# Optimization experiments

Measured on AMD Instinct MI355X. Metric: run time of the kernel, lower is better.

Reference implementation:

```python
import jax, jax.numpy as jnp
import numpy as np

HEADS = 12
WH = WW = 7
N = WH * WW  # 49 tokens per window
NW = 64      # windows per image (mask groups)


def _relative_position_index():
    ch, cw = np.meshgrid(np.arange(WH), np.arange(WW), indexing='ij')
    coords = np.stack([ch, cw]).reshape(2, -1)  # [2, N]
    rel = coords[:, :, None] - coords[:, None, :]  # [2, N, N]
    rel = rel.transpose(1, 2, 0)
    rel[:, :, 0] += WH - 1
    rel[:, :, 1] += WW - 1
    rel[:, :, 0] *= 2 * WW - 1
    return rel.sum(-1).astype(np.int32)  # [N, N]


def setup_inputs() -> dict:
    key = jax.random.key(0)
    ks = jax.random.split(key, 6)
    B, C = 4096, 384
    x = jax.random.normal(ks[0], (B, N, C), dtype=jnp.float32)
    mask = jnp.where(jax.random.uniform(ks[1], (NW, N, N)) > 0.5, 0.0, -100.0).astype(jnp.float32)
    W_qkv = jax.random.normal(ks[2], (C, 3 * C), dtype=jnp.float32) * 0.02
    b_qkv = jnp.zeros((3 * C,), dtype=jnp.float32)
    W_out = jax.random.normal(ks[3], (C, C), dtype=jnp.float32) * 0.02
    b_out = jnp.zeros((C,), dtype=jnp.float32)
    rpb_table = jax.random.normal(ks[4], ((2 * WH - 1) * (2 * WW - 1), HEADS), dtype=jnp.float32) * 0.01
    rel_index = jnp.asarray(_relative_position_index())
    return {"x": x, "mask": mask, "W_qkv": W_qkv, "b_qkv": b_qkv,
            "W_out": W_out, "b_out": b_out, "rpb_table": rpb_table,
            "rel_index": rel_index}


def reference(x, mask, W_qkv, b_qkv, W_out, b_out, rpb_table, rel_index):
    B, n, C = x.shape
    hd = C // HEADS
    scale = hd ** (-0.5)
    qkv = x @ W_qkv + b_qkv                      # [B, n, 3C]
    q, k, v = jnp.split(qkv, 3, axis=2)
    def heads(t):
        return t.reshape(B, n, HEADS, hd).transpose(0, 2, 1, 3)  # b h n d
    q = heads(q) * scale
    k = heads(k)
    v = heads(v)
    attn = jnp.einsum('bhmc,bhnc->bhmn', q, k)   # [B, h, n, n]
    bias = rpb_table[rel_index.reshape(-1)].reshape(n, n, HEADS).transpose(2, 0, 1)
    attn = attn + bias[None]
    nw = mask.shape[0]
    attn = attn.reshape(B // nw, nw, HEADS, n, n) + mask[None, :, None]
    attn = attn.reshape(B, HEADS, n, n)
    attn = jax.nn.softmax(attn, axis=3)
    out = jnp.einsum('bhmn,bhnc->bhmc', attn, v)  # [B, h, n, d]
    out = out.transpose(0, 2, 1, 3).reshape(B, n, C)
    return out @ W_out + b_out
```

## Files before the change

### kernel.cpp

```cpp
#include <hip/hip_runtime.h>

#define NTOK 49
#define CDIM 384
#define HEADS 12
#define HD 32
#define NWIN 64
#define NQKV 1152
#define SCALE 0.17677669529663687f

typedef __attribute__((ext_vector_type(8))) __bf16 bf16x8;
typedef __attribute__((ext_vector_type(4))) float f32x4;

#define OFF_WQKVT   0ull
#define OFF_WOUTT   884736ull
#define OFF_RPBF    1179648ull
#define OFF_MASKF   1376256ull
#define OFF_QKVB    8555520ull
#define OFF_ATTNOUT 470977536ull
#define OFF_XB      OFF_ATTNOUT

#define TSIZE 77070336ull

__device__ __forceinline__ void async_copy16(__bf16* lds_dst, const __bf16* g_src) {
    __builtin_amdgcn_global_load_lds(
        (const __attribute__((address_space(1))) void*)g_src,
        (__attribute__((address_space(3))) void*)lds_dst,
        16, 0, 0);
}


__global__ void prep_weights(const float* __restrict__ Wqkv, const float* __restrict__ Wout,
                             __bf16* __restrict__ WqkvT, __bf16* __restrict__ WoutT) {
    int idx = blockIdx.x * 256 + threadIdx.x;
    if (idx < NQKV * CDIM) {
        int n = idx / CDIM, k = idx % CDIM;
        WqkvT[idx] = (__bf16)Wqkv[(size_t)k * NQKV + n];
    }
    if (idx < CDIM * CDIM) {
        int n = idx / CDIM, k = idx % CDIM;
        WoutT[idx] = (__bf16)Wout[(size_t)k * CDIM + n];
    }
}

__global__ void prep_frag(const float* __restrict__ rpb, const int* __restrict__ rel,
                          const float* __restrict__ mask,
                          float* __restrict__ rpbF, float* __restrict__ maskF) {
    int idx = blockIdx.x * 256 + threadIdx.x;
    if (idx < 49152) {
        int r = idx & 3, lane = (idx >> 2) & 63, nt = (idx >> 8) & 3, mt = (idx >> 10) & 3, h = idx >> 12;
        int m = mt * 16 + ((lane >> 4) << 2) + r, n = nt * 16 + (lane & 15);
        rpbF[idx] = (m < NTOK && n < NTOK) ? rpb[rel[m * NTOK + n] * HEADS + h] : 0.f;
    } else {
        int i2 = idx - 49152;
        if (i2 < 262144) {
            int r = i2 & 3, lane = (i2 >> 2) & 63, nt = (i2 >> 8) & 3, mt = (i2 >> 10) & 3, w = i2 >> 12;
            int m = mt * 16 + ((lane >> 4) << 2) + r, n = nt * 16 + (lane & 15);
            maskF[i2] = (m < NTOK && n < NTOK) ? mask[(size_t)w * NTOK * NTOK + m * NTOK + n] : 0.f;
        }
    }
}

__global__ __launch_bounds__(256) void prep_xb(const float* __restrict__ x,
                                               __bf16* __restrict__ xb, int total8) {
    int stride = gridDim.x * 256;
    for (int i = blockIdx.x * 256 + threadIdx.x; i < total8; i += stride) {
        float4 a = reinterpret_cast<const float4*>(x)[i * 2];
        float4 b = reinterpret_cast<const float4*>(x)[i * 2 + 1];
        union { __bf16 h[8]; uint4 u; } t;
        t.h[0] = (__bf16)a.x; t.h[1] = (__bf16)a.y; t.h[2] = (__bf16)a.z; t.h[3] = (__bf16)a.w;
        t.h[4] = (__bf16)b.x; t.h[5] = (__bf16)b.y; t.h[6] = (__bf16)b.z; t.h[7] = (__bf16)b.w;
        reinterpret_cast<uint4*>(xb)[i] = t.u;
    }
}


__global__ __launch_bounds__(256, 4) void gemm_qkv(
    const __bf16* __restrict__ xb, const __bf16* __restrict__ WqkvT,
    const float* __restrict__ bqkv, __bf16* __restrict__ qkvb)
{
    __shared__ __attribute__((aligned(16))) __bf16 smem[16384];
    __bf16* As = smem;
    __bf16* Bs = smem + 8192;

    const int cpx  = 14112 >> 3;
    const int lid  = (blockIdx.x & 7) * cpx + (blockIdx.x >> 3);
    const int mblk = lid / 9, nblk = lid % 9;
    const int n0  = nblk * 128;
    const int bm0 = mblk * 128;

    const int tid = threadIdx.x;
    const int wave = tid >> 6, lane = tid & 63;
    const int l15 = lane & 15, l4 = lane >> 4;
    const int wr = wave >> 1, wc = wave & 1;

    f32x4 acc[4][4] = {};

    for (int k0 = 0; k0 < CDIM; k0 += 64) {
#pragma unroll
        for (int j = 0; j < 4; ++j) {
            int c = wave * 4 + j;
            int mt = c >> 1, kk = c & 1;
            const __bf16* sa = xb + (size_t)(bm0 + mt * 16 + l15) * CDIM + k0 + kk * 32 + l4 * 8;
            async_copy16(&As[c * 512], sa);
            const __bf16* sb = WqkvT + (size_t)(n0 + mt * 16 + l15) * CDIM + k0 + kk * 32 + l4 * 8;
            async_copy16(&Bs[c * 512], sb);
        }
        __syncthreads();

#pragma unroll
        for (int kk = 0; kk < 2; ++kk) {
            bf16x8 af[4], bf[4];
#pragma unroll
            for (int mi = 0; mi < 4; ++mi)
                af[mi] = *reinterpret_cast<const bf16x8*>(&As[((wr * 4 + mi) * 2 + kk) * 512 + lane * 8]);
#pragma unroll
            for (int ni = 0; ni < 4; ++ni)
                bf[ni] = *reinterpret_cast<const bf16x8*>(&Bs[((wc * 4 + ni) * 2 + kk) * 512 + lane * 8]);
#pragma unroll
            for (int mi = 0; mi < 4; ++mi)
#pragma unroll
                for (int ni = 0; ni < 4; ++ni)
                    acc[mi][ni] = __builtin_amdgcn_mfma_f32_16x16x32_bf16(af[mi], bf[ni], acc[mi][ni], 0, 0, 0);
        }
        __syncthreads();
    }

    const float scl = (n0 < CDIM) ? SCALE : 1.0f;
    float bias[4];
#pragma unroll
    for (int ni = 0; ni < 4; ++ni)
        bias[ni] = bqkv[n0 + wc * 64 + ni * 16 + l15];

    __bf16* Cs = smem;
#pragma unroll
    for (int mi = 0; mi < 4; ++mi)
#pragma unroll
        for (int ni = 0; ni < 4; ++ni)
#pragma unroll
            for (int r = 0; r < 4; ++r) {
                int row = wr * 64 + mi * 16 + l4 * 4 + r;
                int col = wc * 64 + ni * 16 + l15;
                int byte = (row * 256 + col * 2) ^ (((row >> 2) & 3) << 5);
                *reinterpret_cast<__bf16*>(reinterpret_cast<char*>(Cs) + byte) =
                    (__bf16)((acc[mi][ni][r] + bias[ni]) * scl);
            }
    __syncthreads();

    const int which = n0 / CDIM;
    const int h0    = (n0 % CDIM) >> 5;
    __bf16* tbase = qkvb + (size_t)which * TSIZE;
#pragma unroll
    for (int it = 0; it < 8; ++it) {
        int idx = it * 4096 + tid * 16;
        int row = idx >> 8, bcol = idx & 255;
        int sb = (row * 256 + bcol) ^ (((row >> 2) & 3) << 5);
        uint4 v = *reinterpret_cast<const uint4*>(reinterpret_cast<const char*>(Cs) + sb);
        int grow = bm0 + row;
        int b = grow / NTOK, tok = grow - b * NTOK;
        int col = bcol >> 1;
        int h = h0 + (col >> 5), d = col & 31;
        *reinterpret_cast<uint4*>(&tbase[(((size_t)b * HEADS + h) * NTOK + tok) * HD + d]) = v;
    }
}


__global__ __launch_bounds__(256) void attn(
    const __bf16* __restrict__ qkvb, const float* __restrict__ rpbF,
    const float* __restrict__ maskF, __bf16* __restrict__ attnout)
{
    __shared__ __attribute__((aligned(16))) __bf16 vt[4][32 * 64];
    __shared__ __attribute__((aligned(16))) __bf16 ps[4][2][64][8];
    const int b = blockIdx.x;
    const int tid = threadIdx.x;
    const int wave = tid >> 6, lane = tid & 63;
    const int l15 = lane & 15, l4 = lane >> 4;
    const int h = blockIdx.y * 4 + wave;
    const int w = b & (NWIN - 1);

    const size_t hoff = (((size_t)b * HEADS + h) * NTOK) * HD;
    const __bf16* qb = qkvb + hoff;
    const __bf16* kb = qkvb + TSIZE + hoff;
    const __bf16* vb = qkvb + 2 * TSIZE + hoff;
    const f32x4* rpbF4  = reinterpret_cast<const f32x4*>(rpbF);
    const f32x4* maskF4 = reinterpret_cast<const f32x4*>(maskF);

    {
        const int tokb = lane >> 2;
        const int c8   = (lane & 3) * 8;
#pragma unroll
        for (int i = 0; i < 4; ++i) {
            int tok = i * 16 + tokb;
            bf16x8 vv = *reinterpret_cast<const bf16x8*>(vb + (size_t)tok * HD + c8);
#pragma unroll
            for (int j = 0; j < 8; ++j) {
                int d = c8 + j;
                vt[wave][d * 64 + (tok ^ ((d & 7) << 3))] = vv[j];
            }
        }
    }

    bf16x8 kf[4];
#pragma unroll
    for (int nt = 0; nt < 4; ++nt)
        kf[nt] = *reinterpret_cast<const bf16x8*>(kb + (size_t)(nt * 16 + l15) * HD + l4 * 8);

    for (int mt = 0; mt < 4; ++mt) {
        bf16x8 qf = *reinterpret_cast<const bf16x8*>(qb + (size_t)(mt * 16 + l15) * HD + l4 * 8);

        f32x4 rb[4], mb[4];
#pragma unroll
        for (int nt = 0; nt < 4; ++nt) {
            rb[nt] = rpbF4[((h * 4 + mt) * 4 + nt) * 64 + lane];
            mb[nt] = maskF4[((w * 4 + mt) * 4 + nt) * 64 + lane];
        }

        f32x4 s[4];
#pragma unroll
        for (int nt = 0; nt < 4; ++nt) {
            f32x4 z = {};
            s[nt] = __builtin_amdgcn_mfma_f32_16x16x32_bf16(qf, kf[nt], z, 0, 0, 0);
        }

#pragma unroll
        for (int r = 0; r < 4; ++r) {
            float vals[4];
#pragma unroll
            for (int nt = 0; nt < 4; ++nt) {
                int n = nt * 16 + l15;
                vals[nt] = (n < NTOK) ? (s[nt][r] + rb[nt][r] + mb[nt][r]) : -1e30f;
            }
            float mx = fmaxf(fmaxf(vals[0], vals[1]), fmaxf(vals[2], vals[3]));
            mx = fmaxf(mx, __shfl_xor(mx, 1));
            mx = fmaxf(mx, __shfl_xor(mx, 2));
            mx = fmaxf(mx, __shfl_xor(mx, 4));
            mx = fmaxf(mx, __shfl_xor(mx, 8));
            float e0 = __expf(vals[0] - mx);
            float e1 = __expf(vals[1] - mx);
            float e2 = __expf(vals[2] - mx);
            float e3 = __expf(vals[3] - mx);
            float sum = (e0 + e1) + (e2 + e3);
            sum += __shfl_xor(sum, 1);
            sum += __shfl_xor(sum, 2);
            sum += __shfl_xor(sum, 4);
            sum += __shfl_xor(sum, 8);
            float inv = 1.0f / sum;
            float ev[4] = {e0, e1, e2, e3};
#pragma unroll
            for (int nt = 0; nt < 4; ++nt) {
                int lp = (l4 * 4 + r) + 16 * ((nt & 1) * 2 + (l15 >> 3));
                ps[wave][nt >> 1][lp][l15 & 7] = (__bf16)(ev[nt] * inv);
            }
        }

        f32x4 o[2] = {};
#pragma unroll
        for (int kb2 = 0; kb2 < 2; ++kb2) {
            bf16x8 ap = *reinterpret_cast<const bf16x8*>(&ps[wave][kb2][lane][0]);
#pragma unroll
            for (int dt = 0; dt < 2; ++dt) {
                int d = dt * 16 + l15;
                bf16x8 bv = *reinterpret_cast<const bf16x8*>(
                    &vt[wave][d * 64 + ((kb2 * 32 + l4 * 8) ^ ((l15 & 7) << 3))]);
                o[dt] = __builtin_amdgcn_mfma_f32_16x16x32_bf16(ap, bv, o[dt], 0, 0, 0);
            }
        }
#pragma unroll
        for (int dt = 0; dt < 2; ++dt) {
            int col = h * HD + dt * 16 + l15;
#pragma unroll
            for (int r = 0; r < 4; ++r) {
                int tok = mt * 16 + l4 * 4 + r;
                if (tok < NTOK)
                    attnout[((size_t)b * NTOK + tok) * CDIM + col] = (__bf16)o[dt][r];
            }
        }
    }
}


__global__ __launch_bounds__(256, 4) void out_proj(
    const __bf16* __restrict__ A, const __bf16* __restrict__ WoutT,
    const float* __restrict__ bout, float* __restrict__ out)
{
    __shared__ __attribute__((aligned(16))) __bf16 smem[16384];
    __bf16* As = smem;
    __bf16* Bs = smem + 8192;

    const int cpx  = 4704 >> 3;
    const int lid  = (blockIdx.x & 7) * cpx + (blockIdx.x >> 3);
    const int mblk = lid / 3, nblk = lid % 3;
    const int n0  = nblk * 128;
    const int bm0 = mblk * 128;

    const int tid = threadIdx.x;
    const int wave = tid >> 6, lane = tid & 63;
    const int l15 = lane & 15, l4 = lane >> 4;
    const int wr = wave >> 1, wc = wave & 1;

    f32x4 acc[4][4] = {};

    for (int k0 = 0; k0 < CDIM; k0 += 64) {
#pragma unroll
        for (int j = 0; j < 4; ++j) {
            int c = wave * 4 + j;
            int mt = c >> 1, kk = c & 1;
            const __bf16* sa = A + (size_t)(bm0 + mt * 16 + l15) * CDIM + k0 + kk * 32 + l4 * 8;
            async_copy16(&As[c * 512], sa);
            const __bf16* sb = WoutT + (size_t)(n0 + mt * 16 + l15) * CDIM + k0 + kk * 32 + l4 * 8;
            async_copy16(&Bs[c * 512], sb);
        }
        __syncthreads();

#pragma unroll
        for (int kk = 0; kk < 2; ++kk) {
            bf16x8 af[4], bf[4];
#pragma unroll
            for (int mi = 0; mi < 4; ++mi)
                af[mi] = *reinterpret_cast<const bf16x8*>(&As[((wr * 4 + mi) * 2 + kk) * 512 + lane * 8]);
#pragma unroll
            for (int ni = 0; ni < 4; ++ni)
                bf[ni] = *reinterpret_cast<const bf16x8*>(&Bs[((wc * 4 + ni) * 2 + kk) * 512 + lane * 8]);
#pragma unroll
            for (int mi = 0; mi < 4; ++mi)
#pragma unroll
                for (int ni = 0; ni < 4; ++ni)
                    acc[mi][ni] = __builtin_amdgcn_mfma_f32_16x16x32_bf16(af[mi], bf[ni], acc[mi][ni], 0, 0, 0);
        }
        __syncthreads();
    }

    float bias[4];
#pragma unroll
    for (int ni = 0; ni < 4; ++ni)
        bias[ni] = bout[n0 + wc * 64 + ni * 16 + l15];

#pragma unroll
    for (int mi = 0; mi < 4; ++mi)
#pragma unroll
        for (int ni = 0; ni < 4; ++ni)
#pragma unroll
            for (int r = 0; r < 4; ++r) {
                size_t row = (size_t)bm0 + wr * 64 + mi * 16 + l4 * 4 + r;
                int col = n0 + wc * 64 + ni * 16 + l15;
                out[row * CDIM + col] = acc[mi][ni][r] + bias[ni];
            }
}


extern "C" void kernel_launch(void* const* d_in, const int* in_sizes, int n_in,
                              void* d_out, int out_size, void* d_ws, size_t ws_size,
                              hipStream_t stream) {
    (void)n_in; (void)out_size; (void)ws_size;
    const float* x    = (const float*)d_in[0];
    const float* mask = (const float*)d_in[1];
    const float* Wqkv = (const float*)d_in[2];
    const float* bqkv = (const float*)d_in[3];
    const float* Wout = (const float*)d_in[4];
    const float* bout = (const float*)d_in[5];
    const float* rpb  = (const float*)d_in[6];
    const int*   rel  = (const int*)d_in[7];

    const int B = in_sizes[0] / (NTOK * CDIM);
    const int M = B * NTOK;

    char* ws = (char*)d_ws;
    __bf16* WqkvT   = (__bf16*)(ws + OFF_WQKVT);
    __bf16* WoutT   = (__bf16*)(ws + OFF_WOUTT);
    float*  rpbF    = (float*)(ws + OFF_RPBF);
    float*  maskF   = (float*)(ws + OFF_MASKF);
    __bf16* qkvb    = (__bf16*)(ws + OFF_QKVB);
    __bf16* xb      = (__bf16*)(ws + OFF_XB);
    __bf16* attnout = (__bf16*)(ws + OFF_ATTNOUT);
    float*  out     = (float*)d_out;

    prep_weights<<<(NQKV * CDIM + 255) / 256, 256, 0, stream>>>(Wqkv, Wout, WqkvT, WoutT);
    prep_frag<<<(49152 + 262144) / 256, 256, 0, stream>>>(rpb, rel, mask, rpbF, maskF);
    prep_xb<<<2048, 256, 0, stream>>>(x, xb, M * CDIM / 8);
    gemm_qkv<<<(M / 128) * (NQKV / 128), 256, 0, stream>>>(xb, WqkvT, bqkv, qkvb);
    attn<<<dim3(B, 3), 256, 0, stream>>>(qkvb, rpbF, maskF, attnout);
    out_proj<<<(M / 128) * 3, 256, 0, stream>>>(attnout, WoutT, bout, out);
}
```

Measured before the change: 828.1 us.

## Load V fragments directly into registers and stage attention output via LDS

V is no longer transposed through shared memory. Each lane gathers its MFMA B-operand elements straight from global memory with scalar bf16 loads. The attention output is now collected per block in a padded LDS tile and written out as coalesced 16-byte stores, replacing the scattered 2-byte global stores. This trades strided scalar global loads of V for fewer, wider output stores, and adds one block-wide barrier.

```diff
diff --git a/kernel.cpp b/kernel.cpp
--- a/kernel.cpp
+++ b/kernel.cpp
@@ -168,8 +168,8 @@
     const __bf16* __restrict__ qkvb, const float* __restrict__ rpbF,
     const float* __restrict__ maskF, __bf16* __restrict__ attnout)
 {
-    __shared__ __attribute__((aligned(16))) __bf16 vt[4][32 * 64];
     __shared__ __attribute__((aligned(16))) __bf16 ps[4][2][64][8];
+    __shared__ __attribute__((aligned(16))) __bf16 ot[64 * 136];
     const int b = blockIdx.x;
     const int tid = threadIdx.x;
     const int wave = tid >> 6, lane = tid & 63;
@@ -184,20 +184,16 @@
     const f32x4* rpbF4  = reinterpret_cast<const f32x4*>(rpbF);
     const f32x4* maskF4 = reinterpret_cast<const f32x4*>(maskF);
 
-    {
-        const int tokb = lane >> 2;
-        const int c8   = (lane & 3) * 8;
-#pragma unroll
-        for (int i = 0; i < 4; ++i) {
-            int tok = i * 16 + tokb;
-            bf16x8 vv = *reinterpret_cast<const bf16x8*>(vb + (size_t)tok * HD + c8);
+    bf16x8 vf[2][2];
+#pragma unroll
+    for (int dt = 0; dt < 2; ++dt)
+#pragma unroll
+        for (int kb2 = 0; kb2 < 2; ++kb2)
 #pragma unroll
             for (int j = 0; j < 8; ++j) {
-                int d = c8 + j;
-                vt[wave][d * 64 + (tok ^ ((d & 7) << 3))] = vv[j];
-            }
-        }
-    }
+                int tok = kb2 * 32 + l4 * 8 + j;
+                vf[dt][kb2][j] = vb[(size_t)tok * HD + dt * 16 + l15];
+            }
 
     bf16x8 kf[4];
 #pragma unroll
@@ -257,22 +253,27 @@
         for (int kb2 = 0; kb2 < 2; ++kb2) {
             bf16x8 ap = *reinterpret_cast<const bf16x8*>(&ps[wave][kb2][lane][0]);
 #pragma unroll
-            for (int dt = 0; dt < 2; ++dt) {
-                int d = dt * 16 + l15;
-                bf16x8 bv = *reinterpret_cast<const bf16x8*>(
-                    &vt[wave][d * 64 + ((kb2 * 32 + l4 * 8) ^ ((l15 & 7) << 3))]);
-                o[dt] = __builtin_amdgcn_mfma_f32_16x16x32_bf16(ap, bv, o[dt], 0, 0, 0);
-            }
-        }
-#pragma unroll
-        for (int dt = 0; dt < 2; ++dt) {
-            int col = h * HD + dt * 16 + l15;
+            for (int dt = 0; dt < 2; ++dt)
+                o[dt] = __builtin_amdgcn_mfma_f32_16x16x32_bf16(ap, vf[dt][kb2], o[dt], 0, 0, 0);
+        }
+#pragma unroll
+        for (int dt = 0; dt < 2; ++dt)
 #pragma unroll
             for (int r = 0; r < 4; ++r) {
                 int tok = mt * 16 + l4 * 4 + r;
-                if (tok < NTOK)
-                    attnout[((size_t)b * NTOK + tok) * CDIM + col] = (__bf16)o[dt][r];
-            }
+                ot[tok * 136 + wave * 32 + dt * 16 + l15] = (__bf16)o[dt][r];
+            }
+    }
+    __syncthreads();
+
+#pragma unroll
+    for (int it = 0; it < 4; ++it) {
+        int e = it * 2048 + tid * 8;
+        int row = e >> 7, c2 = e & 127;
+        if (row < NTOK) {
+            uint4 v = *reinterpret_cast<const uint4*>(&ot[row * 136 + c2]);
+            *reinterpret_cast<uint4*>(
+                &attnout[((size_t)b * NTOK + row) * CDIM + blockIdx.y * 128 + c2]) = v;
         }
     }
 }
```

After: 819.4 us. No clear change (-1.1%).
